# Kernel optimization log

Hardware: AMD Instinct MI355X
Metric: run time of the kernel (lower is better)

## Reference

```python
import jax, jax.numpy as jnp
import numpy as np

B, S, D = 2, 1024, 4096
H, KVH = 32, 8
HD = D // H          # 128
N_REP = H // KVH     # 4
R = 2                # LoRA rank


def setup_inputs() -> dict:
    key = jax.random.key(0)
    ks = jax.random.split(key, 10)
    sc = 0.02
    x = jax.random.normal(ks[0], (B, S, D), jnp.float32)
    wq = jax.random.normal(ks[1], (D, H * HD), jnp.float32) * sc
    wk = jax.random.normal(ks[2], (D, KVH * HD), jnp.float32) * sc
    wv = jax.random.normal(ks[3], (D, KVH * HD), jnp.float32) * sc
    wo = jax.random.normal(ks[4], (H * HD, D), jnp.float32) * sc
    lora_q_a = jax.random.normal(ks[5], (D, R), jnp.float32) * sc
    lora_q_b = jax.random.normal(ks[6], (R, H * HD), jnp.float32) * sc
    lora_v_a = jax.random.normal(ks[7], (D, R), jnp.float32) * sc
    lora_v_b = jax.random.normal(ks[8], (R, KVH * HD), jnp.float32) * sc
    # RoPE frequencies: freqs_cis[t, i] = exp(1j * t * 10000^(-2i/HD))
    inv_freq = 1.0 / (10000.0 ** (jnp.arange(0, HD, 2, dtype=jnp.float32) / HD))  # [HD/2]
    t = jnp.arange(S, dtype=jnp.float32)
    ang = jnp.outer(t, inv_freq)                      # [S, HD/2]
    freqs_cos = jnp.cos(ang)
    freqs_sin = jnp.sin(ang)
    # causal additive mask [1, 1, S, S]
    mask = jnp.triu(jnp.full((S, S), -1e9, jnp.float32), k=1)[None, None]
    return {"x": x, "wq": wq, "wk": wk, "wv": wv, "wo": wo,
            "lora_q_a": lora_q_a, "lora_q_b": lora_q_b,
            "lora_v_a": lora_v_a, "lora_v_b": lora_v_b,
            "freqs_cos": freqs_cos, "freqs_sin": freqs_sin,
            "mask": mask, "start_pos": 0}


def _rope(t, cos, sin):
    # t: [B, S, h, HD]; pairs (even, odd) are (real, imag) of complex halves
    b, s, h, hd = t.shape
    tr = t.reshape(b, s, h, hd // 2, 2)
    a, bb = tr[..., 0], tr[..., 1]
    c = cos[None, :, None, :]
    sn = sin[None, :, None, :]
    out = jnp.stack([a * c - bb * sn, a * sn + bb * c], axis=-1)
    return out.reshape(b, s, h, hd)


def reference(x, wq, wk, wv, wo, lora_q_a, lora_q_b, lora_v_a, lora_v_b,
              freqs_cos, freqs_sin, mask, start_pos):
    # projections + LoRA (note: original Lora_layer applies NO scaling in forward)
    xq = x @ wq + (x @ lora_q_a) @ lora_q_b            # [B,S,H*HD]
    xk = x @ wk                                         # [B,S,KVH*HD]
    xv = x @ wv + (x @ lora_v_a) @ lora_v_b             # [B,S,KVH*HD]
    xq = xq.reshape(B, S, H, HD)
    xk = xk.reshape(B, S, KVH, HD)
    xv = xv.reshape(B, S, KVH, HD)
    xq = _rope(xq, freqs_cos, freqs_sin)
    xk = _rope(xk, freqs_cos, freqs_sin)
    # repeat_kv (GQA expansion): [B,S,KVH,HD] -> [B,S,H,HD]
    k = jnp.repeat(xk, N_REP, axis=2)
    v = jnp.repeat(xv, N_REP, axis=2)
    # attention
    scores = jnp.einsum('bshd,bthd->bhst', xq, k) / np.sqrt(HD).astype(np.float32)
    scores = scores + mask
    probs = jax.nn.softmax(scores.astype(jnp.float32), axis=-1).astype(xq.dtype)
    out = jnp.einsum('bhst,bthd->bshd', probs, v)       # [B,S,H,HD]
    out = out.reshape(B, S, H * HD) @ wo                # [B,S,D]
    return out
```

## Files before the change

### kernel.cpp

```cpp
#include <hip/hip_runtime.h>
#include <stdint.h>

#define B_ 2
#define S_ 1024
#define D_ 4096
#define H_ 32
#define KVH_ 8
#define HD_ 128

typedef short short8 __attribute__((ext_vector_type(8)));
typedef float floatx4 __attribute__((ext_vector_type(4)));

__device__ __forceinline__ ushort f2bf(float f) {
  union { float f; uint32_t u; } v; v.f = f;
  return (ushort)((v.u + 0x7FFFu + ((v.u >> 16) & 1u)) >> 16);
}
__device__ __forceinline__ float bf2f(ushort u) {
  union { uint32_t x; float f; } v; v.x = ((uint32_t)u) << 16; return v.f;
}

__device__ __forceinline__ void gload16(const void* g, void* l) {
  __builtin_amdgcn_global_load_lds((__attribute__((address_space(1))) void*)g,
                                   (__attribute__((address_space(3))) void*)l,
                                   16, 0, 0);
}

__global__ __launch_bounds__(256) void k_cvtlora(const float* __restrict__ x,
                                                 const float* __restrict__ qa,
                                                 const float* __restrict__ va,
                                                 ushort* __restrict__ xb,
                                                 float* __restrict__ xa) {
  const int row = blockIdx.x, t = threadIdx.x;
  const float* xr = x + (size_t)row * D_;
  ushort* xo = xb + (size_t)row * D_;
  float a0 = 0, a1 = 0, a2 = 0, a3 = 0;
#pragma unroll
  for (int it = 0; it < 4; it++) {
    const int i = it * 1024 + t * 4;
    float4 v = *(const float4*)(xr + i);
    ushort o4[4] = {f2bf(v.x), f2bf(v.y), f2bf(v.z), f2bf(v.w)};
    *(uint2*)(xo + i) = *(uint2*)o4;
    float4 q0 = *(const float4*)(qa + 2 * i);
    float4 q1 = *(const float4*)(qa + 2 * i + 4);
    float4 w0 = *(const float4*)(va + 2 * i);
    float4 w1 = *(const float4*)(va + 2 * i + 4);
    a0 += v.x * q0.x + v.y * q0.z + v.z * q1.x + v.w * q1.z;
    a1 += v.x * q0.y + v.y * q0.w + v.z * q1.y + v.w * q1.w;
    a2 += v.x * w0.x + v.y * w0.z + v.z * w1.x + v.w * w1.z;
    a3 += v.x * w0.y + v.y * w0.w + v.z * w1.y + v.w * w1.w;
  }
#pragma unroll
  for (int off = 32; off; off >>= 1) {
    a0 += __shfl_down(a0, off, 64);
    a1 += __shfl_down(a1, off, 64);
    a2 += __shfl_down(a2, off, 64);
    a3 += __shfl_down(a3, off, 64);
  }
  __shared__ float red[4][4];
  const int w = t >> 6, lane = t & 63;
  if (lane == 0) { red[w][0] = a0; red[w][1] = a1; red[w][2] = a2; red[w][3] = a3; }
  __syncthreads();
  if (t < 4)
    xa[(size_t)row * 4 + t] = red[0][t] + red[1][t] + red[2][t] + red[3][t];
}

__global__ __launch_bounds__(256) void k_trw2(const float* __restrict__ in0,
                                              const float* __restrict__ in1,
                                              ushort* __restrict__ out0,
                                              ushort* __restrict__ out1,
                                              int in_stride, int out_stride) {
  const float* in = blockIdx.z ? in1 : in0;
  ushort* out = blockIdx.z ? out1 : out0;
  __shared__ float t[64][65];
  const int n0 = blockIdx.x * 64, k0 = blockIdx.y * 64;
  const int c4 = (threadIdx.x & 15) * 4, r = threadIdx.x >> 4;
#pragma unroll
  for (int rr = 0; rr < 64; rr += 16) {
    float4 v = *(const float4*)&in[(size_t)(k0 + r + rr) * in_stride + n0 + c4];
    t[r + rr][c4] = v.x; t[r + rr][c4 + 1] = v.y;
    t[r + rr][c4 + 2] = v.z; t[r + rr][c4 + 3] = v.w;
  }
  __syncthreads();
#pragma unroll
  for (int rr = 0; rr < 64; rr += 16) {
    const int n = r + rr;
    ushort o4[4] = {f2bf(t[c4][n]), f2bf(t[c4 + 1][n]),
                    f2bf(t[c4 + 2][n]), f2bf(t[c4 + 3][n])};
    *(uint2*)&out[(size_t)(n0 + n) * out_stride + k0 + c4] = *(uint2*)o4;
  }
}

#define GBAR __builtin_amdgcn_s_barrier()
#define LGKM0 asm volatile("s_waitcnt lgkmcnt(0)" ::: "memory")
#define LGKM8 asm volatile("s_waitcnt lgkmcnt(8)" ::: "memory")
#define VMCNT0 asm volatile("s_waitcnt vmcnt(0)" ::: "memory")
#define VMCNT2 asm volatile("s_waitcnt vmcnt(2)" ::: "memory")
#define VMCNT6 asm volatile("s_waitcnt vmcnt(6)" ::: "memory")

#define QSTAGE_A(KT) do {                                                    \
    const ushort* gp_ = A + (size_t)(m0 + w * 16 + srow) * Kz + (KT) * 64 + scol; \
    char* lp_ = qlds + ((KT) & 1) * 65536 + w * 2048;                        \
    gload16(gp_, lp_);  gload16(gp_ + 8 * Kz, lp_ + 1024);                   \
  } while (0)

#define QSTAGE_B(U, KT) do {                                                 \
    const ushort* gp_ = Bt + (size_t)(n0 + (U) * 128 + w * 16 + srow) * Kz   \
                          + (KT) * 64 + scol;                                \
    char* lp_ = qlds + ((KT) & 1) * 65536 + 16384 + (U) * 16384 + w * 2048;  \
    gload16(gp_, lp_);  gload16(gp_ + 8 * Kz, lp_ + 1024);                   \
  } while (0)

#define QLOAD_AF(BUF) do {                                                   \
    const char* ab_ = qlds + (BUF) * 65536 + (wr * 64 + lr) * 128;           \
    _Pragma("unroll") for (int fr = 0; fr < 4; fr++)                         \
    _Pragma("unroll") for (int ks = 0; ks < 2; ks++)                         \
      af[fr][ks] = *(const short8*)(ab_ + fr * 2048 + (((ks * 4 + g) * 16) ^ swz)); \
  } while (0)

#define QLOAD_BF(J, BUF) do {                                                \
    const char* bb_ = qlds + (BUF) * 65536 + 16384 + (J) * 16384 + (wc * 32 + lr) * 128; \
    _Pragma("unroll") for (int e = 0; e < 2; e++)                            \
    _Pragma("unroll") for (int ks = 0; ks < 2; ks++)                         \
      bf[e][ks] = *(const short8*)(bb_ + e * 2048 + (((ks * 4 + g) * 16) ^ swz)); \
  } while (0)

#define QMFMA(J) do {                                                        \
    __builtin_amdgcn_s_setprio(1);                                           \
    _Pragma("unroll") for (int fr = 0; fr < 4; fr++)                         \
    _Pragma("unroll") for (int e = 0; e < 2; e++)                            \
    _Pragma("unroll") for (int ks = 0; ks < 2; ks++)                         \
      acc[fr][(J) * 2 + e] = __builtin_amdgcn_mfma_f32_16x16x32_bf16(        \
          af[fr][ks], bf[e][ks], acc[fr][(J) * 2 + e], 0, 0, 0);             \
    __builtin_amdgcn_s_setprio(0);                                           \
  } while (0)

__global__ __launch_bounds__(512, 2) void k_gemmq(const ushort* __restrict__ A,
                                                  const ushort* __restrict__ Bt,
                                                  ushort* __restrict__ xq,
                                                  ushort* __restrict__ Vt,
                                                  const float* __restrict__ xa,
                                                  const float* __restrict__ qb,
                                                  const float* __restrict__ vb) {
  __shared__ char qlds[131072];
  const int flat = blockIdx.y * 16 + blockIdx.x;
  const int swz_id = (flat & 7) * 32 + (flat >> 3);
  const int m0 = (swz_id >> 4) * 128, n0 = (swz_id & 15) * 384;
  const int tid = threadIdx.x, lane = tid & 63, w = tid >> 6;
  const int wr = w >> 2, wc = w & 3;
  const int lr = lane & 15, g = lane >> 4;
  const int swz = (lr & 7) * 16;
  const size_t Kz = 4096;
  const int NK = 64;
  const int srow = lane >> 3;
  const int scol = ((lane & 7) ^ (srow & 7)) * 8;

  floatx4 acc[4][6] = {};
  short8 af[4][2], bf[2][2];

  QSTAGE_A(0); QSTAGE_B(0, 0); QSTAGE_B(1, 0); QSTAGE_B(2, 0);
  QSTAGE_A(1); QSTAGE_B(0, 1); QSTAGE_B(1, 1);
  asm volatile("s_waitcnt vmcnt(10)" ::: "memory");
  GBAR;

  for (int t = 0; t < NK; ++t) {
    const int c = t & 1;
    QLOAD_AF(c); QLOAD_BF(0, c);
    if (t + 1 < NK) QSTAGE_B(2, t + 1);
    LGKM8;
    GBAR; LGKM0; QMFMA(0);
    if (t >= NK - 1) { VMCNT0; }
    else { asm volatile("s_waitcnt vmcnt(10)" ::: "memory"); }
    GBAR;
    QLOAD_BF(1, c);
    if (t + 2 < NK) { QSTAGE_A(t + 2); QSTAGE_B(0, t + 2); }
    GBAR; LGKM0; QMFMA(1);
    if (t >= NK - 2) { VMCNT0; }
    else { asm volatile("s_waitcnt vmcnt(12)" ::: "memory"); }
    GBAR;
    QLOAD_BF(2, c);
    if (t + 2 < NK) QSTAGE_B(1, t + 2);
    GBAR; LGKM0; QMFMA(2);
    if (t >= NK - 2) { VMCNT0; }
    else { asm volatile("s_waitcnt vmcnt(10)" ::: "memory"); }
    GBAR;
  }

#pragma unroll
  for (int fr = 0; fr < 4; fr++) {
    const int mb = m0 + wr * 64 + fr * 16 + g * 4;
    const int bb = mb >> 10, s0 = mb & 1023;
    float4 xa4[4];
#pragma unroll
    for (int r = 0; r < 4; r++) xa4[r] = *(const float4*)&xa[(size_t)(mb + r) * 4];
#pragma unroll
    for (int j = 0; j < 3; j++)
#pragma unroll
      for (int e = 0; e < 2; e++) {
        const int n = n0 + j * 128 + wc * 32 + e * 16 + lr;
        if (n < 5120) {
          const bool lq = (n < 4096);
          float b0 = 0.f, b1 = 0.f;
          if (lq) { b0 = qb[n]; b1 = qb[4096 + n]; }
#pragma unroll
          for (int r = 0; r < 4; r++) {
            float cc = acc[fr][j * 2 + e][r];
            if (lq) cc += xa4[r].x * b0 + xa4[r].y * b1;
            xq[(size_t)(mb + r) * 6144 + n] = f2bf(cc);
          }
        } else {
          const int vcol = n - 5120;
          const float b0 = vb[vcol], b1 = vb[1024 + vcol];
          ushort v4[4];
#pragma unroll
          for (int r = 0; r < 4; r++)
            v4[r] = f2bf(acc[fr][j * 2 + e][r] + xa4[r].z * b0 + xa4[r].w * b1);
          *(uint2*)&Vt[(size_t)((bb * 8 + (vcol >> 7)) * 128 + (vcol & 127)) * 1024 + s0] =
              *(uint2*)v4;
        }
      }
  }
}

#define OSTAGE_A(KT) do {                                                    \
    const ushort* gp_ = A + (size_t)(m0 + w * 16 + srow) * Kz + (KT) * 64 + scol; \
    char* lp_ = olds + ((KT) & 1) * 49152 + w * 2048;                        \
    gload16(gp_, lp_);  gload16(gp_ + 8 * Kz, lp_ + 1024);                   \
  } while (0)

#define OSTAGE_B(U, KT) do {                                                 \
    const ushort* gp_ = Bt + (size_t)(n0 + (U) * 128 + w * 16 + srow) * Kz   \
                          + (KT) * 64 + scol;                                \
    char* lp_ = olds + ((KT) & 1) * 49152 + 16384 + (U) * 16384 + w * 2048;  \
    gload16(gp_, lp_);  gload16(gp_ + 8 * Kz, lp_ + 1024);                   \
  } while (0)

#define OLOAD_AF(BUF) do {                                                   \
    const char* ab_ = olds + (BUF) * 49152 + (wr * 64 + lr) * 128;           \
    _Pragma("unroll") for (int fr = 0; fr < 4; fr++)                         \
    _Pragma("unroll") for (int ks = 0; ks < 2; ks++)                         \
      af[fr][ks] = *(const short8*)(ab_ + fr * 2048 + (((ks * 4 + g) * 16) ^ swz)); \
  } while (0)

#define OLOAD_BF(U, BUF) do {                                                \
    const char* bb_ = olds + (BUF) * 49152 + 16384 + (U) * 16384 + (wc * 32 + lr) * 128; \
    _Pragma("unroll") for (int e = 0; e < 2; e++)                            \
    _Pragma("unroll") for (int ks = 0; ks < 2; ks++)                         \
      bf[e][ks] = *(const short8*)(bb_ + e * 2048 + (((ks * 4 + g) * 16) ^ swz)); \
  } while (0)

#define OMFMA(U) do {                                                        \
    __builtin_amdgcn_s_setprio(1);                                           \
    _Pragma("unroll") for (int fr = 0; fr < 4; fr++)                         \
    _Pragma("unroll") for (int e = 0; e < 2; e++)                            \
    _Pragma("unroll") for (int ks = 0; ks < 2; ks++)                         \
      acc[fr][(U) * 2 + e] = __builtin_amdgcn_mfma_f32_16x16x32_bf16(        \
          af[fr][ks], bf[e][ks], acc[fr][(U) * 2 + e], 0, 0, 0);             \
    __builtin_amdgcn_s_setprio(0);                                           \
  } while (0)

__global__ __launch_bounds__(512, 2) void k_gemmo(const ushort* __restrict__ A,
                                                  const ushort* __restrict__ Bt,
                                                  float* __restrict__ C) {
  __shared__ char olds[98304];
  const int flat = blockIdx.y * 16 + blockIdx.x;
  const int swz_id = (flat & 7) * 32 + (flat >> 3);
  const int m0 = (swz_id >> 4) * 128, n0 = (swz_id & 15) * 256;
  const int tid = threadIdx.x, lane = tid & 63, w = tid >> 6;
  const int wr = w >> 2, wc = w & 3;
  const int lr = lane & 15, g = lane >> 4;
  const int swz = (lr & 7) * 16;
  const size_t Kz = 4096;
  const int NK = 64;
  const int srow = lane >> 3;
  const int scol = ((lane & 7) ^ (srow & 7)) * 8;

  floatx4 acc[4][4] = {};
  short8 af[4][2], bf[2][2];

  OSTAGE_A(0); OSTAGE_B(0, 0); OSTAGE_B(1, 0);
  OSTAGE_A(1); OSTAGE_B(0, 1);
  asm volatile("s_waitcnt vmcnt(4)" ::: "memory");
  GBAR;

  for (int t = 0; t < NK; ++t) {
    const int c = t & 1;
    OLOAD_AF(c); OLOAD_BF(0, c);
    if (t + 1 < NK) OSTAGE_B(1, t + 1);
    LGKM8;
    GBAR; LGKM0; OMFMA(0);
    if (t == NK - 1) { VMCNT0; } else { VMCNT6; }
    GBAR;
    OLOAD_BF(1, c);
    if (t + 2 < NK) { OSTAGE_A(t + 2); OSTAGE_B(0, t + 2); }
    GBAR; LGKM0; OMFMA(1);
    if (t < NK - 2) { VMCNT6; }
    else if (t == NK - 2) { VMCNT2; }
    GBAR;
  }

#pragma unroll
  for (int fr = 0; fr < 4; fr++) {
    const int mb = m0 + wr * 64 + fr * 16 + g * 4;
#pragma unroll
    for (int j = 0; j < 2; j++)
#pragma unroll
      for (int e = 0; e < 2; e++) {
        const int n = n0 + j * 128 + wc * 32 + e * 16 + lr;
#pragma unroll
        for (int r = 0; r < 4; r++)
          C[(size_t)(mb + r) * 4096 + n] = acc[fr][j * 2 + e][r];
      }
  }
}

__global__ __launch_bounds__(256) void k_rope(const ushort* __restrict__ xq,
                                              const float* __restrict__ fcos,
                                              const float* __restrict__ fsin,
                                              ushort* __restrict__ Qb,
                                              ushort* __restrict__ Kb) {
  const int s = blockIdx.x, b = blockIdx.y;
  const ushort* row = xq + (size_t)(b * S_ + s) * 6144;
#pragma unroll
  for (int it = 0; it < 8; it++) {
    int p2 = it * 256 + threadIdx.x;
    int h = p2 >> 6, p = p2 & 63;
    uint32_t u = *(const uint32_t*)(row + h * 128 + 2 * p);
    float a = bf2f((ushort)u), bb = bf2f((ushort)(u >> 16));
    float c = fcos[s * 64 + p], sn = fsin[s * 64 + p];
    uint32_t pk = (uint32_t)f2bf(a * c - bb * sn) |
                  ((uint32_t)f2bf(a * sn + bb * c) << 16);
    *(uint32_t*)(Qb + ((size_t)(b * H_ + h) * S_ + s) * HD_ + 2 * p) = pk;
  }
#pragma unroll
  for (int it = 0; it < 2; it++) {
    int p2 = it * 256 + threadIdx.x;
    int h = p2 >> 6, p = p2 & 63;
    uint32_t u = *(const uint32_t*)(row + 4096 + h * 128 + 2 * p);
    float a = bf2f((ushort)u), bb = bf2f((ushort)(u >> 16));
    float c = fcos[s * 64 + p], sn = fsin[s * 64 + p];
    uint32_t pk = (uint32_t)f2bf(a * c - bb * sn) |
                  ((uint32_t)f2bf(a * sn + bb * c) << 16);
    *(uint32_t*)(Kb + ((size_t)(b * KVH_ + h) * S_ + s) * HD_ + 2 * p) = pk;
  }
}

#define FSTAGE(T, DB) do {                                                   \
    _Pragma("unroll") for (int i_ = 0; i_ < 4; i_++) {                       \
      gload16(Kg + (size_t)((T) * 64 + i_ * 16 + k_srow) * HD_ + k_scol,     \
              fls + (DB) * 16384 + i_ * 4096 + w * 1024);                    \
      gload16(Vg + (size_t)(i_ * 32 + v_srow) * S_ + (T) * 64 + v_scol,      \
              fls + 32768 + (DB) * 16384 + i_ * 4096 + w * 1024);            \
    }                                                                        \
  } while (0)

__global__ __launch_bounds__(256, 2) void k_flash(const ushort* __restrict__ Qb,
                                                  const ushort* __restrict__ Kb,
                                                  const ushort* __restrict__ Vt,
                                                  ushort* __restrict__ attn) {
  __shared__ char fls[81920];
  const int qblk = (gridDim.x - 1) - blockIdx.x;
  const int h = blockIdx.y, b = blockIdx.z;
  const int kvh = h >> 2;
  const int tid = threadIdx.x, w = tid >> 6, lane = tid & 63;
  const int lr = lane & 15, g = lane >> 4;
  const int swz = (lr & 7) * 16;
  const int qra = qblk * 128 + w * 16;
  const ushort* Qrow = Qb + ((size_t)(b * H_ + h) * S_ + qra + lr) * HD_;
  short8 qfa[4], qfb[4];
#pragma unroll
  for (int ks = 0; ks < 4; ks++) {
    qfa[ks] = *(const short8*)(Qrow + ks * 32 + g * 8);
    qfb[ks] = *(const short8*)(Qrow + 64 * HD_ + ks * 32 + g * 8);
  }
  const ushort* Kg = Kb + (size_t)(b * KVH_ + kvh) * S_ * HD_;
  const ushort* Vg = Vt + (size_t)(b * KVH_ + kvh) * HD_ * S_;
  char* Pw = fls + 65536 + w * 4096;
  const int q7 = lr & 7;
  const int k_srow = tid >> 4;
  const int k_scol = ((tid & 15) ^ (k_srow & 7)) * 8;
  const int v_srow = tid >> 3;
  const int v_scol = ((tid & 7) ^ (v_srow & 7)) * 8;
  const float scale = 0.088388347648318447f;

  float m_a = -1e30f, l_a = 0.f, m_b = -1e30f, l_b = 0.f;
  floatx4 oa[8] = {}, ob[8] = {};
  const int nt = 2 * qblk + 2;
  const int lastA = 2 * qblk;

  FSTAGE(0, 0);
  VMCNT0;
  GBAR;

  for (int t = 0; t < nt; t++) {
    const int cur = t & 1;
    if (t + 1 < nt) FSTAGE(t + 1, cur ^ 1);
    const char* Kl = fls + cur * 16384;
    const char* Vl = fls + 32768 + cur * 16384;
    if (t <= lastA) {
      floatx4 s4[4] = {};
      __builtin_amdgcn_s_setprio(1);
#pragma unroll
      for (int mf = 0; mf < 4; mf++) {
        const char* Krow = Kl + (mf * 16 + lr) * 256;
#pragma unroll
        for (int ks = 0; ks < 4; ks++) {
          short8 kf = *(const short8*)(Krow + (((ks * 4 + g) * 16) ^ swz));
          s4[mf] = __builtin_amdgcn_mfma_f32_16x16x32_bf16(kf, qfa[ks], s4[mf], 0, 0, 0);
        }
      }
      __builtin_amdgcn_s_setprio(0);
      float tm = -1e30f;
      if (t == lastA) {
#pragma unroll
        for (int mf = 0; mf < 4; mf++)
#pragma unroll
          for (int r = 0; r < 4; r++) {
            int kv = t * 64 + mf * 16 + g * 4 + r;
            float v = (kv > qra + lr) ? -1e30f : s4[mf][r] * scale;
            s4[mf][r] = v; tm = fmaxf(tm, v);
          }
      } else {
#pragma unroll
        for (int mf = 0; mf < 4; mf++)
#pragma unroll
          for (int r = 0; r < 4; r++) {
            float v = s4[mf][r] * scale;
            s4[mf][r] = v; tm = fmaxf(tm, v);
          }
      }
      tm = fmaxf(tm, __shfl_xor(tm, 16, 64));
      tm = fmaxf(tm, __shfl_xor(tm, 32, 64));
      float m_new = fmaxf(m_a, tm);
      float corr = __expf(m_a - m_new);
      float rs = 0.f;
#pragma unroll
      for (int mf = 0; mf < 4; mf++)
#pragma unroll
        for (int r = 0; r < 4; r++) {
          float p = __expf(s4[mf][r] - m_new);
          s4[mf][r] = p; rs += p;
        }
      rs += __shfl_xor(rs, 16, 64);
      rs += __shfl_xor(rs, 32, 64);
      l_a = l_a * corr + rs; m_a = m_new;
#pragma unroll
      for (int r = 0; r < 4; r++) {
        float cr = __shfl(corr, g * 4 + r, 64);
#pragma unroll
        for (int nf = 0; nf < 8; nf++) oa[nf][r] *= cr;
      }
#pragma unroll
      for (int mf = 0; mf < 4; mf++) {
        uint2 pv;
        pv.x = (uint32_t)f2bf(s4[mf][0]) | ((uint32_t)f2bf(s4[mf][1]) << 16);
        pv.y = (uint32_t)f2bf(s4[mf][2]) | ((uint32_t)f2bf(s4[mf][3]) << 16);
        *(uint2*)(Pw + lr * 128 + ((mf * 32 + g * 8) ^ (q7 << 4))) = pv;
      }
    }
    {
      floatx4 s4[4] = {};
      __builtin_amdgcn_s_setprio(1);
#pragma unroll
      for (int mf = 0; mf < 4; mf++) {
        const char* Krow = Kl + (mf * 16 + lr) * 256;
#pragma unroll
        for (int ks = 0; ks < 4; ks++) {
          short8 kf = *(const short8*)(Krow + (((ks * 4 + g) * 16) ^ swz));
          s4[mf] = __builtin_amdgcn_mfma_f32_16x16x32_bf16(kf, qfb[ks], s4[mf], 0, 0, 0);
        }
      }
      __builtin_amdgcn_s_setprio(0);
      float tm = -1e30f;
      if (t == nt - 1) {
#pragma unroll
        for (int mf = 0; mf < 4; mf++)
#pragma unroll
          for (int r = 0; r < 4; r++) {
            int kv = t * 64 + mf * 16 + g * 4 + r;
            float v = (kv > qra + 64 + lr) ? -1e30f : s4[mf][r] * scale;
            s4[mf][r] = v; tm = fmaxf(tm, v);
          }
      } else {
#pragma unroll
        for (int mf = 0; mf < 4; mf++)
#pragma unroll
          for (int r = 0; r < 4; r++) {
            float v = s4[mf][r] * scale;
            s4[mf][r] = v; tm = fmaxf(tm, v);
          }
      }
      tm = fmaxf(tm, __shfl_xor(tm, 16, 64));
      tm = fmaxf(tm, __shfl_xor(tm, 32, 64));
      float m_new = fmaxf(m_b, tm);
      float corr = __expf(m_b - m_new);
      float rs = 0.f;
#pragma unroll
      for (int mf = 0; mf < 4; mf++)
#pragma unroll
        for (int r = 0; r < 4; r++) {
          float p = __expf(s4[mf][r] - m_new);
          s4[mf][r] = p; rs += p;
        }
      rs += __shfl_xor(rs, 16, 64);
      rs += __shfl_xor(rs, 32, 64);
      l_b = l_b * corr + rs; m_b = m_new;
#pragma unroll
      for (int r = 0; r < 4; r++) {
        float cr = __shfl(corr, g * 4 + r, 64);
#pragma unroll
        for (int nf = 0; nf < 8; nf++) ob[nf][r] *= cr;
      }
#pragma unroll
      for (int mf = 0; mf < 4; mf++) {
        uint2 pv;
        pv.x = (uint32_t)f2bf(s4[mf][0]) | ((uint32_t)f2bf(s4[mf][1]) << 16);
        pv.y = (uint32_t)f2bf(s4[mf][2]) | ((uint32_t)f2bf(s4[mf][3]) << 16);
        *(uint2*)(Pw + 2048 + lr * 128 + ((mf * 32 + g * 8) ^ (q7 << 4))) = pv;
      }
    }
    __builtin_amdgcn_s_setprio(1);
#pragma unroll
    for (int ks2 = 0; ks2 < 2; ks2++) {
      short8 pb = *(const short8*)(Pw + 2048 + lr * 128 + ((ks2 * 64 + g * 16) ^ (q7 << 4)));
      short8 pa = pb;
      if (t <= lastA)
        pa = *(const short8*)(Pw + lr * 128 + ((ks2 * 64 + g * 16) ^ (q7 << 4)));
#pragma unroll
      for (int nf = 0; nf < 8; nf++) {
        short8 vf = *(const short8*)(Vl + (nf * 16 + lr) * 128 + (((ks2 * 4 + g) * 16) ^ swz));
        if (t <= lastA)
          oa[nf] = __builtin_amdgcn_mfma_f32_16x16x32_bf16(pa, vf, oa[nf], 0, 0, 0);
        ob[nf] = __builtin_amdgcn_mfma_f32_16x16x32_bf16(pb, vf, ob[nf], 0, 0, 0);
      }
    }
    __builtin_amdgcn_s_setprio(0);
    VMCNT0;
    GBAR;
  }
  const float linva = 1.0f / l_a, linvb = 1.0f / l_b;
  ushort* outp = attn + ((size_t)(b * S_) + qra) * 4096 + h * 128;
#pragma unroll
  for (int r = 0; r < 4; r++) {
    float lia = __shfl(linva, g * 4 + r, 64);
    float lib = __shfl(linvb, g * 4 + r, 64);
    ushort* orow = outp + (size_t)(g * 4 + r) * 4096;
#pragma unroll
    for (int nf = 0; nf < 8; nf++) {
      orow[nf * 16 + lr] = f2bf(oa[nf][r] * lia);
      orow[(size_t)64 * 4096 + nf * 16 + lr] = f2bf(ob[nf][r] * lib);
    }
  }
}

extern "C" void kernel_launch(void* const* d_in, const int* in_sizes, int n_in,
                              void* d_out, int out_size, void* d_ws, size_t ws_size,
                              hipStream_t stream) {
  (void)in_sizes; (void)n_in; (void)out_size; (void)ws_size;
  const float* x    = (const float*)d_in[0];
  const float* wq   = (const float*)d_in[1];
  const float* wk   = (const float*)d_in[2];
  const float* wv   = (const float*)d_in[3];
  const float* wo   = (const float*)d_in[4];
  const float* lqa  = (const float*)d_in[5];
  const float* lqb  = (const float*)d_in[6];
  const float* lva  = (const float*)d_in[7];
  const float* lvb  = (const float*)d_in[8];
  const float* fcos = (const float*)d_in[9];
  const float* fsin = (const float*)d_in[10];

  char* ws = (char*)d_ws;
  ushort* xb   = (ushort*)(ws + 0);
  ushort* wT   = (ushort*)(ws + 16777216);
  ushort* woT  = (ushort*)(ws + 67108864);
  ushort* xq   = (ushort*)(ws + 100663296);
  ushort* Qb   = (ushort*)(ws + 150994944);
  ushort* Kb   = (ushort*)(ws + 167772160);
  ushort* Vt   = (ushort*)(ws + 171966464);
  ushort* attn = (ushort*)(ws + 176160768);
  float*  xa   = (float*) (ws + 192937984);

  k_cvtlora<<<2048, 256, 0, stream>>>(x, lqa, lva, xb, xa);
  k_trw2<<<dim3(64, 64, 2), 256, 0, stream>>>(wq, wo, wT, woT, 4096, 4096);
  k_trw2<<<dim3(16, 64, 2), 256, 0, stream>>>(wk, wv, wT + (size_t)4096 * 4096,
                                              wT + (size_t)5120 * 4096, 1024, 4096);
  k_gemmq<<<dim3(16, 16), 512, 0, stream>>>(xb, wT, xq, Vt, xa, lqb, lvb);
  k_rope<<<dim3(1024, 2), 256, 0, stream>>>(xq, fcos, fsin, Qb, Kb);
  k_flash<<<dim3(8, 32, 2), 256, 0, stream>>>(Qb, Kb, Vt, attn);
  k_gemmo<<<dim3(16, 16), 512, 0, stream>>>(attn, woT, (float*)d_out);
}
```

Baseline: 301.9 us.

## Restructure Q and O GEMM mainloops into triple-buffered single-barrier pipelines

Both projection GEMMs move from a double-buffered LDS pipeline with several barriers and sub-stage staging per K-step to a three-buffer ring. Each K-tile issues the prefetch two tiles ahead, loads all fragments, runs every MFMA for the tile, then waits and syncs once. The Q GEMM also halves its K-tile to 32 with a new 4-way swizzle, which cuts LDS to 96KB but doubles the iteration count. The O GEMM grows to 144KB LDS. The aim is fewer barriers and more latency hiding, at the cost of LDS footprint and possibly occupancy for the O kernel.

```diff
diff --git a/kernel.cpp b/kernel.cpp
--- a/kernel.cpp
+++ b/kernel.cpp
@@ -91,47 +91,36 @@
 }
 
 #define GBAR __builtin_amdgcn_s_barrier()
-#define LGKM0 asm volatile("s_waitcnt lgkmcnt(0)" ::: "memory")
-#define LGKM8 asm volatile("s_waitcnt lgkmcnt(8)" ::: "memory")
 #define VMCNT0 asm volatile("s_waitcnt vmcnt(0)" ::: "memory")
-#define VMCNT2 asm volatile("s_waitcnt vmcnt(2)" ::: "memory")
+#define VMCNT4 asm volatile("s_waitcnt vmcnt(4)" ::: "memory")
 #define VMCNT6 asm volatile("s_waitcnt vmcnt(6)" ::: "memory")
 
-#define QSTAGE_A(KT) do {                                                    \
-    const ushort* gp_ = A + (size_t)(m0 + w * 16 + srow) * Kz + (KT) * 64 + scol; \
-    char* lp_ = qlds + ((KT) & 1) * 65536 + w * 2048;                        \
-    gload16(gp_, lp_);  gload16(gp_ + 8 * Kz, lp_ + 1024);                   \
+#define QSTG(T, SB) do {                                                     \
+    const ushort* ga_ = A + (size_t)(m0 + srow) * Kz + (T) * 32 + ssl;       \
+    gload16(ga_, qlds + (SB) * 32768 + w * 1024);                            \
+    _Pragma("unroll") for (int u_ = 0; u_ < 3; u_++) {                       \
+      const ushort* gb_ = Bt + (size_t)(n0 + u_ * 128 + srow) * Kz + (T) * 32 + ssl; \
+      gload16(gb_, qlds + (SB) * 32768 + 8192 + u_ * 8192 + w * 1024);       \
+    }                                                                        \
   } while (0)
 
-#define QSTAGE_B(U, KT) do {                                                 \
-    const ushort* gp_ = Bt + (size_t)(n0 + (U) * 128 + w * 16 + srow) * Kz   \
-                          + (KT) * 64 + scol;                                \
-    char* lp_ = qlds + ((KT) & 1) * 65536 + 16384 + (U) * 16384 + w * 2048;  \
-    gload16(gp_, lp_);  gload16(gp_ + 8 * Kz, lp_ + 1024);                   \
-  } while (0)
-
-#define QLOAD_AF(BUF) do {                                                   \
-    const char* ab_ = qlds + (BUF) * 65536 + (wr * 64 + lr) * 128;           \
+#define QTILE(T, RB) do {                                                    \
+    if ((T) + 2 < 128) QSTG((T) + 2, ((RB) + 2) % 3);                        \
+    const char* ab_ = qlds + (RB) * 32768 + (wr * 64 + lr) * 64 + ((g ^ (lr & 3)) << 4); \
     _Pragma("unroll") for (int fr = 0; fr < 4; fr++)                         \
-    _Pragma("unroll") for (int ks = 0; ks < 2; ks++)                         \
-      af[fr][ks] = *(const short8*)(ab_ + fr * 2048 + (((ks * 4 + g) * 16) ^ swz)); \
-  } while (0)
-
-#define QLOAD_BF(J, BUF) do {                                                \
-    const char* bb_ = qlds + (BUF) * 65536 + 16384 + (J) * 16384 + (wc * 32 + lr) * 128; \
-    _Pragma("unroll") for (int e = 0; e < 2; e++)                            \
-    _Pragma("unroll") for (int ks = 0; ks < 2; ks++)                         \
-      bf[e][ks] = *(const short8*)(bb_ + e * 2048 + (((ks * 4 + g) * 16) ^ swz)); \
-  } while (0)
-
-#define QMFMA(J) do {                                                        \
+      af[fr] = *(const short8*)(ab_ + fr * 1024);                            \
+    const char* bb_ = qlds + (RB) * 32768 + 8192 + (wc * 32 + lr) * 64 + ((g ^ (lr & 3)) << 4); \
+    _Pragma("unroll") for (int u_ = 0; u_ < 3; u_++)                         \
+    _Pragma("unroll") for (int e_ = 0; e_ < 2; e_++)                         \
+      bfr[u_ * 2 + e_] = *(const short8*)(bb_ + u_ * 8192 + e_ * 1024);      \
     __builtin_amdgcn_s_setprio(1);                                           \
     _Pragma("unroll") for (int fr = 0; fr < 4; fr++)                         \
-    _Pragma("unroll") for (int e = 0; e < 2; e++)                            \
-    _Pragma("unroll") for (int ks = 0; ks < 2; ks++)                         \
-      acc[fr][(J) * 2 + e] = __builtin_amdgcn_mfma_f32_16x16x32_bf16(        \
-          af[fr][ks], bf[e][ks], acc[fr][(J) * 2 + e], 0, 0, 0);             \
+    _Pragma("unroll") for (int u_ = 0; u_ < 6; u_++)                         \
+      acc[fr][u_] = __builtin_amdgcn_mfma_f32_16x16x32_bf16(                 \
+          af[fr], bfr[u_], acc[fr][u_], 0, 0, 0);                            \
     __builtin_amdgcn_s_setprio(0);                                           \
+    if ((T) + 2 < 128) { VMCNT4; } else { VMCNT0; }                          \
+    GBAR;                                                                    \
   } while (0)
 
 __global__ __launch_bounds__(512, 2) void k_gemmq(const ushort* __restrict__ A,
@@ -141,49 +130,31 @@
                                                   const float* __restrict__ xa,
                                                   const float* __restrict__ qb,
                                                   const float* __restrict__ vb) {
-  __shared__ char qlds[131072];
+  __shared__ char qlds[98304];
   const int flat = blockIdx.y * 16 + blockIdx.x;
   const int swz_id = (flat & 7) * 32 + (flat >> 3);
   const int m0 = (swz_id >> 4) * 128, n0 = (swz_id & 15) * 384;
   const int tid = threadIdx.x, lane = tid & 63, w = tid >> 6;
   const int wr = w >> 2, wc = w & 3;
   const int lr = lane & 15, g = lane >> 4;
-  const int swz = (lr & 7) * 16;
   const size_t Kz = 4096;
-  const int NK = 64;
-  const int srow = lane >> 3;
-  const int scol = ((lane & 7) ^ (srow & 7)) * 8;
+  const int srow = tid >> 2;
+  const int ssl = ((tid & 3) ^ (srow & 3)) * 8;
 
   floatx4 acc[4][6] = {};
-  short8 af[4][2], bf[2][2];
-
-  QSTAGE_A(0); QSTAGE_B(0, 0); QSTAGE_B(1, 0); QSTAGE_B(2, 0);
-  QSTAGE_A(1); QSTAGE_B(0, 1); QSTAGE_B(1, 1);
-  asm volatile("s_waitcnt vmcnt(10)" ::: "memory");
+  short8 af[4], bfr[6];
+
+  QSTG(0, 0); QSTG(1, 1);
+  VMCNT4;
   GBAR;
 
-  for (int t = 0; t < NK; ++t) {
-    const int c = t & 1;
-    QLOAD_AF(c); QLOAD_BF(0, c);
-    if (t + 1 < NK) QSTAGE_B(2, t + 1);
-    LGKM8;
-    GBAR; LGKM0; QMFMA(0);
-    if (t >= NK - 1) { VMCNT0; }
-    else { asm volatile("s_waitcnt vmcnt(10)" ::: "memory"); }
-    GBAR;
-    QLOAD_BF(1, c);
-    if (t + 2 < NK) { QSTAGE_A(t + 2); QSTAGE_B(0, t + 2); }
-    GBAR; LGKM0; QMFMA(1);
-    if (t >= NK - 2) { VMCNT0; }
-    else { asm volatile("s_waitcnt vmcnt(12)" ::: "memory"); }
-    GBAR;
-    QLOAD_BF(2, c);
-    if (t + 2 < NK) QSTAGE_B(1, t + 2);
-    GBAR; LGKM0; QMFMA(2);
-    if (t >= NK - 2) { VMCNT0; }
-    else { asm volatile("s_waitcnt vmcnt(10)" ::: "memory"); }
-    GBAR;
-  }
+  for (int tt = 0; tt < 126; tt += 3) {
+    QTILE(tt + 0, 0);
+    QTILE(tt + 1, 1);
+    QTILE(tt + 2, 2);
+  }
+  QTILE(126, 0);
+  QTILE(127, 1);
 
 #pragma unroll
   for (int fr = 0; fr < 4; fr++) {
@@ -221,47 +192,43 @@
   }
 }
 
-#define OSTAGE_A(KT) do {                                                    \
-    const ushort* gp_ = A + (size_t)(m0 + w * 16 + srow) * Kz + (KT) * 64 + scol; \
-    char* lp_ = olds + ((KT) & 1) * 49152 + w * 2048;                        \
-    gload16(gp_, lp_);  gload16(gp_ + 8 * Kz, lp_ + 1024);                   \
+#define OSTG(T, SB) do {                                                     \
+    const ushort* ga_ = A + (size_t)(m0 + w * 16 + osr) * Kz + (T) * 64 + osc; \
+    char* la_ = olds + (SB) * 49152 + w * 2048;                              \
+    gload16(ga_, la_); gload16(ga_ + 8 * Kz, la_ + 1024);                    \
+    _Pragma("unroll") for (int u_ = 0; u_ < 2; u_++) {                       \
+      const ushort* gb_ = Bt + (size_t)(n0 + u_ * 128 + w * 16 + osr) * Kz + (T) * 64 + osc; \
+      char* lb_ = olds + (SB) * 49152 + 16384 + u_ * 16384 + w * 2048;       \
+      gload16(gb_, lb_); gload16(gb_ + 8 * Kz, lb_ + 1024);                  \
+    }                                                                        \
   } while (0)
 
-#define OSTAGE_B(U, KT) do {                                                 \
-    const ushort* gp_ = Bt + (size_t)(n0 + (U) * 128 + w * 16 + srow) * Kz   \
-                          + (KT) * 64 + scol;                                \
-    char* lp_ = olds + ((KT) & 1) * 49152 + 16384 + (U) * 16384 + w * 2048;  \
-    gload16(gp_, lp_);  gload16(gp_ + 8 * Kz, lp_ + 1024);                   \
-  } while (0)
-
-#define OLOAD_AF(BUF) do {                                                   \
-    const char* ab_ = olds + (BUF) * 49152 + (wr * 64 + lr) * 128;           \
+#define OTILE(T, RB) do {                                                    \
+    if ((T) + 2 < 64) OSTG((T) + 2, ((RB) + 2) % 3);                         \
+    const char* ab_ = olds + (RB) * 49152 + (wr * 64 + lr) * 128;            \
     _Pragma("unroll") for (int fr = 0; fr < 4; fr++)                         \
     _Pragma("unroll") for (int ks = 0; ks < 2; ks++)                         \
       af[fr][ks] = *(const short8*)(ab_ + fr * 2048 + (((ks * 4 + g) * 16) ^ swz)); \
-  } while (0)
-
-#define OLOAD_BF(U, BUF) do {                                                \
-    const char* bb_ = olds + (BUF) * 49152 + 16384 + (U) * 16384 + (wc * 32 + lr) * 128; \
-    _Pragma("unroll") for (int e = 0; e < 2; e++)                            \
+    const char* bb_ = olds + (RB) * 49152 + 16384 + (wc * 32 + lr) * 128;    \
+    _Pragma("unroll") for (int u_ = 0; u_ < 2; u_++)                         \
+    _Pragma("unroll") for (int e_ = 0; e_ < 2; e_++)                         \
     _Pragma("unroll") for (int ks = 0; ks < 2; ks++)                         \
-      bf[e][ks] = *(const short8*)(bb_ + e * 2048 + (((ks * 4 + g) * 16) ^ swz)); \
-  } while (0)
-
-#define OMFMA(U) do {                                                        \
+      bfr[u_ * 2 + e_][ks] = *(const short8*)(bb_ + u_ * 16384 + e_ * 2048 + (((ks * 4 + g) * 16) ^ swz)); \
     __builtin_amdgcn_s_setprio(1);                                           \
     _Pragma("unroll") for (int fr = 0; fr < 4; fr++)                         \
-    _Pragma("unroll") for (int e = 0; e < 2; e++)                            \
+    _Pragma("unroll") for (int u_ = 0; u_ < 4; u_++)                         \
     _Pragma("unroll") for (int ks = 0; ks < 2; ks++)                         \
-      acc[fr][(U) * 2 + e] = __builtin_amdgcn_mfma_f32_16x16x32_bf16(        \
-          af[fr][ks], bf[e][ks], acc[fr][(U) * 2 + e], 0, 0, 0);             \
+      acc[fr][u_] = __builtin_amdgcn_mfma_f32_16x16x32_bf16(                 \
+          af[fr][ks], bfr[u_][ks], acc[fr][u_], 0, 0, 0);                    \
     __builtin_amdgcn_s_setprio(0);                                           \
+    if ((T) + 2 < 64) { VMCNT6; } else { VMCNT0; }                           \
+    GBAR;                                                                    \
   } while (0)
 
 __global__ __launch_bounds__(512, 2) void k_gemmo(const ushort* __restrict__ A,
                                                   const ushort* __restrict__ Bt,
                                                   float* __restrict__ C) {
-  __shared__ char olds[98304];
+  __shared__ char olds[147456];
   const int flat = blockIdx.y * 16 + blockIdx.x;
   const int swz_id = (flat & 7) * 32 + (flat >> 3);
   const int m0 = (swz_id >> 4) * 128, n0 = (swz_id & 15) * 256;
@@ -270,33 +237,22 @@
   const int lr = lane & 15, g = lane >> 4;
   const int swz = (lr & 7) * 16;
   const size_t Kz = 4096;
-  const int NK = 64;
-  const int srow = lane >> 3;
-  const int scol = ((lane & 7) ^ (srow & 7)) * 8;
+  const int osr = lane >> 3;
+  const int osc = ((lane & 7) ^ (osr & 7)) * 8;
 
   floatx4 acc[4][4] = {};
-  short8 af[4][2], bf[2][2];
-
-  OSTAGE_A(0); OSTAGE_B(0, 0); OSTAGE_B(1, 0);
-  OSTAGE_A(1); OSTAGE_B(0, 1);
-  asm volatile("s_waitcnt vmcnt(4)" ::: "memory");
+  short8 af[4][2], bfr[4][2];
+
+  OSTG(0, 0); OSTG(1, 1);
+  VMCNT6;
   GBAR;
 
-  for (int t = 0; t < NK; ++t) {
-    const int c = t & 1;
-    OLOAD_AF(c); OLOAD_BF(0, c);
-    if (t + 1 < NK) OSTAGE_B(1, t + 1);
-    LGKM8;
-    GBAR; LGKM0; OMFMA(0);
-    if (t == NK - 1) { VMCNT0; } else { VMCNT6; }
-    GBAR;
-    OLOAD_BF(1, c);
-    if (t + 2 < NK) { OSTAGE_A(t + 2); OSTAGE_B(0, t + 2); }
-    GBAR; LGKM0; OMFMA(1);
-    if (t < NK - 2) { VMCNT6; }
-    else if (t == NK - 2) { VMCNT2; }
-    GBAR;
-  }
+  for (int tt = 0; tt < 63; tt += 3) {
+    OTILE(tt + 0, 0);
+    OTILE(tt + 1, 1);
+    OTILE(tt + 2, 2);
+  }
+  OTILE(63, 0);
 
 #pragma unroll
   for (int fr = 0; fr < 4; fr++) {
```

After: 308.6 us. +2.2%, slower.
